# Performance work log

Measured on AMD Instinct MI355X. Metric: run time of the kernel, lower is better.

Reference implementation:

```python
import jax, jax.numpy as jnp
import numpy as np

NLON = 720  # output longitude points for irfft
B, C = 4, 8
LMAX, MMAX, NLAT = 360, 361, 361


def setup_inputs() -> dict:
    key = jax.random.key(0)
    kx, kd = jax.random.split(key)
    # x: real view of complex coeffs, shape [B, C, 2(vec comp), lmax, mmax, 2(re/im)]
    x = jax.random.normal(kx, (B, C, 2, LMAX, MMAX, 2), dtype=jnp.float32)
    # dpct: precomputed dLegendre buffer, shape [2, mmax, lmax, nlat]
    dpct = jax.random.normal(kd, (2, MMAX, LMAX, NLAT), dtype=jnp.float32) * 0.1
    return {"x": x, "dpct": dpct}


def reference(x, dpct):
    # split vector components and real/imag parts
    x0r = x[..., 0, :, :, 0]  # [..., lmax, mmax]
    x0i = x[..., 0, :, :, 1]
    x1r = x[..., 1, :, :, 0]
    x1i = x[..., 1, :, :, 1]
    d0 = dpct[0].astype(x.dtype)  # [mmax, lmax, nlat]
    d1 = dpct[1].astype(x.dtype)

    def ein(a, d):
        return jnp.einsum('...lm,mlk->...km', a, d)

    srl = ein(x0r, d0) - ein(x1i, d1)   # [..., nlat, mmax]
    sim = ein(x0i, d0) + ein(x1r, d1)
    trl = -ein(x0i, d1) - ein(x1r, d0)
    tim = ein(x0r, d1) - ein(x1i, d0)

    s = jax.lax.complex(srl, sim)
    t = jax.lax.complex(trl, tim)
    xs = jnp.stack((s, t), axis=-3)     # [..., 2, nlat, mmax] complex
    # inverse real FFT over longitude, 'forward' norm (no scaling on inverse)
    out = jnp.fft.irfft(xs, n=NLON, axis=-1, norm='forward')  # [..., 2, nlat, nlon]
    return out
```

## Files before the change

### kernel.cpp

```cpp
#include <hip/hip_runtime.h>
#include <hip/hip_bf16.h>
#include <math.h>

#define LMAX 360
#define MMAX 361
#define NLAT 361
#define NLON 720
#define BC   32
#define MT   (BC*2*NLAT)
#define NLATP 364
#define MTP  (BC*2*NLATP)
#define QT   722
#define KP   736
#define NP   768
#define BM   128
#define BN   128
#define BK   32

typedef __attribute__((ext_vector_type(8))) short short8;
typedef __attribute__((ext_vector_type(4))) short short4v;
typedef __attribute__((ext_vector_type(4))) float f32x4;

static __device__ __forceinline__ short f2bf(float v) {
    __hip_bfloat16 h = __float2bfloat16(v);
    return *reinterpret_cast<short*>(&h);
}

__global__ __launch_bounds__(256) void sht_prep_x(
    const float* __restrict__ x, __hip_bfloat16* __restrict__ xT)
{
    const int m0 = blockIdx.x * 32;
    const int l0 = blockIdx.y * 64;
    const int bc = blockIdx.z >> 1, f = blockIdx.z & 1;
    __shared__ float2 tile[64][33];
    const float2* __restrict__ x2 = (const float2*)x;
    const int t = threadIdx.x;
    const int rm = t & 31, rl = t >> 5;

    const int mm = min(m0 + rm, MMAX - 1);
    #pragma unroll
    for (int r = 0; r < 8; ++r) {
        int l = min(l0 + rl + r * 8, LMAX - 1);
        tile[rl + r * 8][rm] = x2[((size_t)(bc * 2 + f) * LMAX + l) * MMAX + mm];
    }
    __syncthreads();

    const int tm = t >> 3, lg = t & 7;
    const int m = m0 + tm;
    if (m >= MMAX) return;
    const int lw = l0 + lg * 8;
    if (lw >= LMAX) return;

    short8 re, im;
    #pragma unroll
    for (int e = 0; e < 8; ++e) {
        float2 v = tile[lg * 8 + e][tm];
        re[e] = f2bf(v.x);
        im[e] = f2bf(v.y);
    }
    size_t mb = (size_t)m * (128 * LMAX);
    *(short8*)((short*)xT + mb + (size_t)((f * 2 + 0) * 32 + bc) * LMAX + lw) = re;
    *(short8*)((short*)xT + mb + (size_t)((f * 2 + 1) * 32 + bc) * LMAX + lw) = im;
}

__global__ __launch_bounds__(256, 3) void sht_gemm1(
    const float* __restrict__ dpct, const __hip_bfloat16* __restrict__ xT,
    __hip_bfloat16* __restrict__ interQ)
{
    const int m  = blockIdx.y;
    const int K0 = blockIdx.x * 96;

    __shared__ __align__(16) char AlsB[96 * 128];
    __shared__ __align__(16) char BlsB[128 * 128];

    const int t    = threadIdx.x;
    const int lane = t & 63;
    const int wave = t >> 6;
    const int wm = (wave >> 1) * 48;
    const int wn = (wave & 1) * 64;
    const int fr = lane & 15;
    const int lq = lane >> 4;

    int kdv[3], lov[3], kcl[3];
    #pragma unroll
    for (int it = 0; it < 3; ++it) {
        int task = it * 256 + t;
        kdv[it] = task % 96;
        lov[it] = task / 96;
        kcl[it] = min(K0 + kdv[it], 360);
    }
    const int cB    = t >> 1;
    const int plane = cB >> 5, bcq = cB & 31;
    const int g0B   = (t & 1) * 4;

    const int            srcT[8] = {0, 1, 2, 3, 3, 2, 1, 0};
    const unsigned short sgnT[8] = {0, 0, 0x8000, 0x8000, 0x8000, 0, 0x8000, 0};

    f32x4 acc[3][4];
    const f32x4 zero = {0.f, 0.f, 0.f, 0.f};
    #pragma unroll
    for (int i = 0; i < 3; ++i)
        #pragma unroll
        for (int j = 0; j < 4; ++j) acc[i][j] = zero;

    float a0_[3][8], a1_[3][8];
    bool  v0_[3],    v1_[3];
    short8 bpf[4];
    bool   bvB[4];
    short  bsgn = 0;

#define STEP_P(s)  ((s) >= 6 ? 1 : 0)
#define STEP_L(s)  (((s) % 6) * 64)

#define LOAD_A(AP, LV, ss) {                                                   \
    const int p_ = STEP_P(ss); const int l0_ = STEP_L(ss);                     \
    const size_t rowb_ = ((size_t)p_ * MMAX + m) * LMAX;                       \
    _Pragma("unroll")                                                          \
    for (int it = 0; it < 3; ++it) {                                           \
        int lb_ = l0_ + lov[it] * 8;                                           \
        LV[it] = (lb_ < LMAX);                                                 \
        int lcl_ = LV[it] ? lb_ : 0;                                           \
        const float* sp_ = dpct + (rowb_ + lcl_) * (size_t)NLAT + kcl[it];     \
        _Pragma("unroll")                                                      \
        for (int e = 0; e < 8; ++e)                                            \
            AP[it][e] = sp_[(size_t)e * NLAT];                                 \
    } }

#define LOAD_B(ss) {                                                           \
    const int p_ = STEP_P(ss); const int l0_ = STEP_L(ss);                     \
    int src_ = srcT[p_ * 4 + plane];                                           \
    bsgn = (short)sgnT[p_ * 4 + plane];                                        \
    const short* bb_ = (const short*)xT + (size_t)m * (128 * LMAX) +           \
                       (size_t)(src_ * 32 + bcq) * LMAX;                       \
    _Pragma("unroll")                                                          \
    for (int i = 0; i < 4; ++i) {                                              \
        int lg2_ = l0_ + (g0B + i) * 8;                                        \
        bvB[i] = (lg2_ < LMAX);                                                \
        int lcl_ = bvB[i] ? lg2_ : 0;                                          \
        bpf[i] = *(const short8*)(bb_ + lcl_);                                 \
    } }

#define WRITE_A(AP, LV) {                                                      \
    _Pragma("unroll")                                                          \
    for (int it = 0; it < 3; ++it) {                                           \
        short8 w_;                                                             \
        _Pragma("unroll")                                                      \
        for (int e = 0; e < 8; ++e)                                            \
            w_[e] = LV[it] ? f2bf(AP[it][e]) : (short)0;                       \
        int kd_ = kdv[it], lo_ = lov[it];                                      \
        *(short8*)(AlsB + kd_ * 128 + ((lo_ ^ (kd_ & 7)) << 4)) = w_;          \
    } }

#define WRITE_B() {                                                            \
    _Pragma("unroll")                                                          \
    for (int i = 0; i < 4; ++i) {                                              \
        short8 v_ = bpf[i];                                                    \
        _Pragma("unroll")                                                      \
        for (int e = 0; e < 8; ++e) {                                          \
            short xe_ = (short)(v_[e] ^ bsgn);                                 \
            v_[e] = bvB[i] ? xe_ : (short)0;                                   \
        }                                                                      \
        int g_ = g0B + i;                                                      \
        *(short8*)(BlsB + cB * 128 + ((g_ ^ (cB & 7)) << 4)) = v_;             \
    } }

    auto compute = [&]() {
        #pragma unroll
        for (int kk = 0; kk < 2; ++kk) {
            short8 af[3], bg[4];
            const int g = kk * 4 + lq;
            #pragma unroll
            for (int mi = 0; mi < 3; ++mi) {
                int k = wm + mi * 16 + fr;
                af[mi] = *(const short8*)(AlsB + k * 128 + ((g ^ (k & 7)) << 4));
            }
            #pragma unroll
            for (int ni = 0; ni < 4; ++ni) {
                int c = wn + ni * 16 + fr;
                bg[ni] = *(const short8*)(BlsB + c * 128 + ((g ^ (c & 7)) << 4));
            }
            #pragma unroll
            for (int mi = 0; mi < 3; ++mi)
                #pragma unroll
                for (int ni = 0; ni < 4; ++ni)
                    acc[mi][ni] = __builtin_amdgcn_mfma_f32_16x16x32_bf16(
                        af[mi], bg[ni], acc[mi][ni], 0, 0, 0);
        }
    };

    LOAD_B(0);
    LOAD_A(a0_, v0_, 0);
    LOAD_A(a1_, v1_, 1);

    #pragma unroll 1
    for (int s = 0; s < 12; s += 2) {
        __syncthreads();
        WRITE_A(a0_, v0_);
        WRITE_B();
        __syncthreads();
        if (s + 1 < 12) LOAD_B(s + 1);
        if (s + 2 < 12) LOAD_A(a0_, v0_, s + 2);
        compute();

        __syncthreads();
        WRITE_A(a1_, v1_);
        WRITE_B();
        __syncthreads();
        if (s + 2 < 12) LOAD_B(s + 2);
        if (s + 3 < 12) LOAD_A(a1_, v1_, s + 3);
        compute();
    }

#undef LOAD_A
#undef LOAD_B
#undef WRITE_A
#undef WRITE_B
#undef STEP_P
#undef STEP_L

    #pragma unroll
    for (int mi = 0; mi < 3; ++mi) {
        int kr = K0 + wm + mi * 16 + lq * 4;
        #pragma unroll
        for (int ni = 0; ni < 4; ++ni) {
            int c = wn + ni * 16 + fr;
            int pl = c >> 5, bc = c & 31;
            int ri = pl & 1, tt = pl >> 1;
            size_t qb = (size_t)(2 * m + ri) * MTP + (size_t)(bc * 2 + tt) * NLATP;
            if (kr + 3 <= 360) {
                short4v w;
                #pragma unroll
                for (int r = 0; r < 4; ++r) w[r] = f2bf(acc[mi][ni][r]);
                *(short4v*)((short*)interQ + qb + kr) = w;
            } else if (kr <= 360) {
                ((short*)interQ)[qb + kr] = f2bf(acc[mi][ni][0]);
            }
        }
    }
}

__global__ __launch_bounds__(256) void sht_transpose(
    const __hip_bfloat16* __restrict__ inQ, __hip_bfloat16* __restrict__ outT)
{
    __shared__ __hip_bfloat16 tile[64][65];
    const int R0 = blockIdx.x * 64;
    const int q0 = blockIdx.y * 64;
    const int tx = threadIdx.x & 63;
    const int ty = threadIdx.x >> 6;
    const __hip_bfloat16 zv = __float2bfloat16(0.f);

    const int R  = R0 + tx;
    const int Rm = (R / NLAT) * NLATP + (R % NLAT);

    for (int qq = ty; qq < 64; qq += 4) {
        int q = q0 + qq;
        tile[qq][tx] = (q < QT) ? inQ[(size_t)q * MTP + Rm] : zv;
    }
    __syncthreads();
    if (q0 + tx < KP) {
        for (int rr = ty; rr < 64; rr += 4) {
            outT[(size_t)(R0 + rr) * KP + q0 + tx] = tile[tx][rr];
        }
    }
}

__global__ __launch_bounds__(256) void sht_make_w(__hip_bfloat16* __restrict__ W)
{
    const int idx = blockIdx.x * 256 + threadIdx.x;
    const int j = idx / KP;
    const int q = idx % KP;
    float v = 0.f;
    if (j < NLON && q < QT) {
        int m = q >> 1;
        float coef = (m == 0 || m == 360) ? 1.f : 2.f;
        int ph = (m * j) % 720;
        float ang = (float)ph * (float)(2.0 * M_PI / 720.0);
        float s, c;
        __sincosf(ang, &s, &c);
        v = (q & 1) ? (-coef * s) : (coef * c);
    }
    W[idx] = __float2bfloat16(v);
}

__global__ __launch_bounds__(256) void sht_gemm(
    const __hip_bfloat16* __restrict__ A,
    const __hip_bfloat16* __restrict__ W,
    float* __restrict__ out)
{
    __shared__ __align__(16) __hip_bfloat16 As[BM * BK];
    __shared__ __align__(16) __hip_bfloat16 Bs[BN * BK];
    const int t  = threadIdx.x;
    const int R0 = blockIdx.x * BM;
    const int J0 = blockIdx.y * BN;

    const int rowA = t >> 2;
    const int kc   = (t & 3) * 8;
    const int gr0  = min(R0 + rowA,      MT - 1);
    const int gr1  = min(R0 + rowA + 64, MT - 1);
    const __hip_bfloat16* pa0 = A + (size_t)gr0 * KP + kc;
    const __hip_bfloat16* pa1 = A + (size_t)gr1 * KP + kc;
    const __hip_bfloat16* pb0 = W + (size_t)(J0 + rowA) * KP + kc;
    const __hip_bfloat16* pb1 = W + (size_t)(J0 + rowA + 64) * KP + kc;

    const int lane = t & 63;
    const int wave = t >> 6;
    const int wm = (wave >> 1) * 64;
    const int wn = (wave & 1) * 64;
    const int fr = lane & 15;
    const int kg = (lane >> 4) * 8;

    f32x4 acc[4][4];
    const f32x4 zero = {0.f, 0.f, 0.f, 0.f};
    #pragma unroll
    for (int i = 0; i < 4; ++i)
        #pragma unroll
        for (int j = 0; j < 4; ++j) acc[i][j] = zero;

    short8 va0 = *(const short8*)pa0;
    short8 va1 = *(const short8*)pa1;
    short8 vb0 = *(const short8*)pb0;
    short8 vb1 = *(const short8*)pb1;

    for (int kt = 0; kt < KP / BK; ++kt) {
        __syncthreads();
        *(short8*)&As[t * 8]        = va0;
        *(short8*)&As[t * 8 + 2048] = va1;
        *(short8*)&Bs[t * 8]        = vb0;
        *(short8*)&Bs[t * 8 + 2048] = vb1;
        __syncthreads();

        if (kt + 1 < KP / BK) {
            const int ko = (kt + 1) * BK;
            va0 = *(const short8*)(pa0 + ko);
            va1 = *(const short8*)(pa1 + ko);
            vb0 = *(const short8*)(pb0 + ko);
            vb1 = *(const short8*)(pb1 + ko);
        }

        short8 af[4], bg[4];
        #pragma unroll
        for (int i = 0; i < 4; ++i)
            af[i] = *(const short8*)&As[(wm + i * 16 + fr) * BK + kg];
        #pragma unroll
        for (int i = 0; i < 4; ++i)
            bg[i] = *(const short8*)&Bs[(wn + i * 16 + fr) * BK + kg];

        #pragma unroll
        for (int mi = 0; mi < 4; ++mi)
            #pragma unroll
            for (int ni = 0; ni < 4; ++ni)
                acc[mi][ni] = __builtin_amdgcn_mfma_f32_16x16x32_bf16(
                    af[mi], bg[ni], acc[mi][ni], 0, 0, 0);
    }

    const int orow = (lane >> 4) * 4;
    #pragma unroll
    for (int mi = 0; mi < 4; ++mi) {
        #pragma unroll
        for (int ni = 0; ni < 4; ++ni) {
            #pragma unroll
            for (int r = 0; r < 4; ++r) {
                int row = R0 + wm + mi * 16 + orow + r;
                int col = J0 + wn + ni * 16 + fr;
                if (row < MT && col < NLON)
                    out[(size_t)row * NLON + col] = acc[mi][ni][r];
            }
        }
    }
}

extern "C" void kernel_launch(void* const* d_in, const int* in_sizes, int n_in,
                              void* d_out, int out_size, void* d_ws, size_t ws_size,
                              hipStream_t stream)
{
    const float* x    = (const float*)d_in[0];
    const float* dpct = (const float*)d_in[1];
    float* out        = (float*)d_out;

    char* ws = (char*)d_ws;
    __hip_bfloat16* xT     = (__hip_bfloat16*)ws;
    __hip_bfloat16* interT = (__hip_bfloat16*)(ws + 34009088);
    __hip_bfloat16* interQ = (__hip_bfloat16*)(ws + 70254592);
    __hip_bfloat16* Wt     = (__hip_bfloat16*)(ws + 104857600);

    dim3 gp(12, 6, 64);
    sht_prep_x<<<gp, 256, 0, stream>>>(x, xT);

    dim3 g1(4, MMAX);
    sht_gemm1<<<g1, 256, 0, stream>>>(dpct, xT, interQ);

    dim3 gt(MT / 64, 12);
    sht_transpose<<<gt, 256, 0, stream>>>(interQ, interT);

    sht_make_w<<<(NP * KP) / 256, 256, 0, stream>>>(Wt);

    dim3 gg((MT + BM - 1) / BM, NP / BN);
    sht_gemm<<<gg, 256, 0, stream>>>(interT, Wt, out);
}
```

Before: 312.8 us.

## Reuse x tile across both Legendre planes and drop padded intermediate layout

The first GEMM now loads each x chunk into shared memory once per l-chunk and reuses it for both dpct planes. The plane-dependent row permutation and sign flip move from the staging write into the MFMA fragment read, where they are applied with an XOR. This roughly halves global and shared-memory traffic for the B operand, at the cost of extra VALU work and index arithmetic in the inner compute loop. The padded NLATP intermediate layout is removed, so the epilogue falls back to scalar bf16 stores. Workspace buffers are also aliased (interT over xT, Wt over interQ) to shrink the footprint.

New measurement: 343.2 us. 9.7% more time.

```diff
diff --git a/kernel.cpp b/kernel.cpp
--- a/kernel.cpp
+++ b/kernel.cpp
@@ -8,8 +8,6 @@
 #define NLON 720
 #define BC   32
 #define MT   (BC*2*NLAT)
-#define NLATP 364
-#define MTP  (BC*2*NLATP)
 #define QT   722
 #define KP   736
 #define NP   768
@@ -18,7 +16,6 @@
 #define BK   32
 
 typedef __attribute__((ext_vector_type(8))) short short8;
-typedef __attribute__((ext_vector_type(4))) short short4v;
 typedef __attribute__((ext_vector_type(4))) float f32x4;
 
 static __device__ __forceinline__ short f2bf(float v) {
@@ -89,9 +86,8 @@
         lov[it] = task / 96;
         kcl[it] = min(K0 + kdv[it], 360);
     }
-    const int cB    = t >> 1;
-    const int plane = cB >> 5, bcq = cB & 31;
-    const int g0B   = (t & 1) * 4;
+    const int cB  = t >> 1;
+    const int g0B = (t & 1) * 4;
 
     const int            srcT[8] = {0, 1, 2, 3, 3, 2, 1, 0};
     const unsigned short sgnT[8] = {0, 0, 0x8000, 0x8000, 0x8000, 0, 0x8000, 0};
@@ -107,14 +103,10 @@
     bool  v0_[3],    v1_[3];
     short8 bpf[4];
     bool   bvB[4];
-    short  bsgn = 0;
-
-#define STEP_P(s)  ((s) >= 6 ? 1 : 0)
-#define STEP_L(s)  (((s) % 6) * 64)
-
-#define LOAD_A(AP, LV, ss) {                                                   \
-    const int p_ = STEP_P(ss); const int l0_ = STEP_L(ss);                     \
-    const size_t rowb_ = ((size_t)p_ * MMAX + m) * LMAX;                       \
+
+#define LOAD_A(AP, LV, pp, lc) {                                               \
+    const int l0_ = (lc) * 64;                                                 \
+    const size_t rowb_ = ((size_t)(pp) * MMAX + m) * LMAX;                     \
     _Pragma("unroll")                                                          \
     for (int it = 0; it < 3; ++it) {                                           \
         int lb_ = l0_ + lov[it] * 8;                                           \
@@ -126,12 +118,10 @@
             AP[it][e] = sp_[(size_t)e * NLAT];                                 \
     } }
 
-#define LOAD_B(ss) {                                                           \
-    const int p_ = STEP_P(ss); const int l0_ = STEP_L(ss);                     \
-    int src_ = srcT[p_ * 4 + plane];                                           \
-    bsgn = (short)sgnT[p_ * 4 + plane];                                        \
+#define LOAD_B(lc) {                                                           \
+    const int l0_ = (lc) * 64;                                                 \
     const short* bb_ = (const short*)xT + (size_t)m * (128 * LMAX) +           \
-                       (size_t)(src_ * 32 + bcq) * LMAX;                       \
+                       (size_t)cB * LMAX;                                      \
     _Pragma("unroll")                                                          \
     for (int i = 0; i < 4; ++i) {                                              \
         int lg2_ = l0_ + (g0B + i) * 8;                                        \
@@ -156,67 +146,65 @@
     for (int i = 0; i < 4; ++i) {                                              \
         short8 v_ = bpf[i];                                                    \
         _Pragma("unroll")                                                      \
-        for (int e = 0; e < 8; ++e) {                                          \
-            short xe_ = (short)(v_[e] ^ bsgn);                                 \
-            v_[e] = bvB[i] ? xe_ : (short)0;                                   \
-        }                                                                      \
+        for (int e = 0; e < 8; ++e) v_[e] = bvB[i] ? v_[e] : (short)0;         \
         int g_ = g0B + i;                                                      \
         *(short8*)(BlsB + cB * 128 + ((g_ ^ (cB & 7)) << 4)) = v_;             \
     } }
 
-    auto compute = [&]() {
-        #pragma unroll
-        for (int kk = 0; kk < 2; ++kk) {
-            short8 af[3], bg[4];
-            const int g = kk * 4 + lq;
-            #pragma unroll
-            for (int mi = 0; mi < 3; ++mi) {
-                int k = wm + mi * 16 + fr;
-                af[mi] = *(const short8*)(AlsB + k * 128 + ((g ^ (k & 7)) << 4));
-            }
-            #pragma unroll
-            for (int ni = 0; ni < 4; ++ni) {
-                int c = wn + ni * 16 + fr;
-                bg[ni] = *(const short8*)(BlsB + c * 128 + ((g ^ (c & 7)) << 4));
-            }
-            #pragma unroll
-            for (int mi = 0; mi < 3; ++mi)
-                #pragma unroll
-                for (int ni = 0; ni < 4; ++ni)
-                    acc[mi][ni] = __builtin_amdgcn_mfma_f32_16x16x32_bf16(
-                        af[mi], bg[ni], acc[mi][ni], 0, 0, 0);
-        }
-    };
+#define COMPUTE(AF_SRC, pp) {                                                  \
+    _Pragma("unroll")                                                          \
+    for (int kk = 0; kk < 2; ++kk) {                                           \
+        const int g = kk * 4 + lq;                                             \
+        short8 af[3];                                                          \
+        _Pragma("unroll")                                                      \
+        for (int mi = 0; mi < 3; ++mi) {                                       \
+            int k = wm + mi * 16 + fr;                                         \
+            af[mi] = *(const short8*)(AlsB + k * 128 + ((g ^ (k & 7)) << 4));  \
+        }                                                                      \
+        _Pragma("unroll")                                                      \
+        for (int ni = 0; ni < 4; ++ni) {                                       \
+            int pl_ = 2 * (wave & 1) + (ni >> 1);                              \
+            int rB_ = srcT[(pp) * 4 + pl_] * 32 + (ni & 1) * 16 + fr;          \
+            short8 bg = *(const short8*)(                                      \
+                BlsB + rB_ * 128 + ((g ^ (rB_ & 7)) << 4));                    \
+            short sg_ = (short)sgnT[(pp) * 4 + pl_];                           \
+            _Pragma("unroll")                                                  \
+            for (int e = 0; e < 8; ++e) bg[e] ^= sg_;                          \
+            _Pragma("unroll")                                                  \
+            for (int mi = 0; mi < 3; ++mi)                                     \
+                acc[mi][ni] = __builtin_amdgcn_mfma_f32_16x16x32_bf16(         \
+                    af[mi], bg, acc[mi][ni], 0, 0, 0);                         \
+        }                                                                      \
+    } }
 
     LOAD_B(0);
-    LOAD_A(a0_, v0_, 0);
-    LOAD_A(a1_, v1_, 1);
+    LOAD_A(a0_, v0_, 0, 0);
+    LOAD_A(a1_, v1_, 1, 0);
 
     #pragma unroll 1
-    for (int s = 0; s < 12; s += 2) {
-        __syncthreads();
+    for (int lc = 0; lc < 6; ++lc) {
+        __syncthreads();
+        WRITE_B();
         WRITE_A(a0_, v0_);
-        WRITE_B();
-        __syncthreads();
-        if (s + 1 < 12) LOAD_B(s + 1);
-        if (s + 2 < 12) LOAD_A(a0_, v0_, s + 2);
-        compute();
+        __syncthreads();
+        if (lc < 5) {
+            LOAD_B(lc + 1);
+            LOAD_A(a0_, v0_, 0, lc + 1);
+        }
+        COMPUTE(a0_, 0);
 
         __syncthreads();
         WRITE_A(a1_, v1_);
-        WRITE_B();
-        __syncthreads();
-        if (s + 2 < 12) LOAD_B(s + 2);
-        if (s + 3 < 12) LOAD_A(a1_, v1_, s + 3);
-        compute();
+        __syncthreads();
+        if (lc < 5) LOAD_A(a1_, v1_, 1, lc + 1);
+        COMPUTE(a1_, 1);
     }
 
 #undef LOAD_A
 #undef LOAD_B
 #undef WRITE_A
 #undef WRITE_B
-#undef STEP_P
-#undef STEP_L
+#undef COMPUTE
 
     #pragma unroll
     for (int mi = 0; mi < 3; ++mi) {
@@ -226,14 +214,12 @@
             int c = wn + ni * 16 + fr;
             int pl = c >> 5, bc = c & 31;
             int ri = pl & 1, tt = pl >> 1;
-            size_t qb = (size_t)(2 * m + ri) * MTP + (size_t)(bc * 2 + tt) * NLATP;
-            if (kr + 3 <= 360) {
-                short4v w;
-                #pragma unroll
-                for (int r = 0; r < 4; ++r) w[r] = f2bf(acc[mi][ni][r]);
-                *(short4v*)((short*)interQ + qb + kr) = w;
-            } else if (kr <= 360) {
-                ((short*)interQ)[qb + kr] = f2bf(acc[mi][ni][0]);
+            size_t qb = (size_t)(2 * m + ri) * MT + (size_t)(bc * 2 + tt) * NLAT;
+            #pragma unroll
+            for (int r = 0; r < 4; ++r) {
+                int k = kr + r;
+                if (k < NLAT)
+                    interQ[qb + k] = __float2bfloat16(acc[mi][ni][r]);
             }
         }
     }
@@ -249,12 +235,9 @@
     const int ty = threadIdx.x >> 6;
     const __hip_bfloat16 zv = __float2bfloat16(0.f);
 
-    const int R  = R0 + tx;
-    const int Rm = (R / NLAT) * NLATP + (R % NLAT);
-
     for (int qq = ty; qq < 64; qq += 4) {
         int q = q0 + qq;
-        tile[qq][tx] = (q < QT) ? inQ[(size_t)q * MTP + Rm] : zv;
+        tile[qq][tx] = (q < QT) ? inQ[(size_t)q * MT + R0 + tx] : zv;
     }
     __syncthreads();
     if (q0 + tx < KP) {
@@ -379,9 +362,9 @@
 
     char* ws = (char*)d_ws;
     __hip_bfloat16* xT     = (__hip_bfloat16*)ws;
-    __hip_bfloat16* interT = (__hip_bfloat16*)(ws + 34009088);
-    __hip_bfloat16* interQ = (__hip_bfloat16*)(ws + 70254592);
-    __hip_bfloat16* Wt     = (__hip_bfloat16*)(ws + 104857600);
+    __hip_bfloat16* interT = (__hip_bfloat16*)ws;
+    __hip_bfloat16* interQ = (__hip_bfloat16*)(ws + 34009088);
+    __hip_bfloat16* Wt     = (__hip_bfloat16*)(ws + 34009088);
 
     dim3 gp(12, 6, 64);
     sht_prep_x<<<gp, 256, 0, stream>>>(x, xT);
```
